# Kernel tuning notes

Hardware: AMD Instinct MI355X
Metric: run time of the kernel (lower is better)

## Reference

```python
import jax, jax.numpy as jnp
import numpy as np

B, T, D, H = 4, 1024, 1024, 16
HD = D // H
DFF = 2048          # ExpertTier hidden width
K = 3               # ConvTier causal kernel size
NEG = -1e9


def layernorm(x, w, b, eps=1e-5):
    m = jnp.mean(x, axis=-1, keepdims=True)
    v = jnp.var(x, axis=-1, keepdims=True)
    return (x - m) * jax.lax.rsqrt(v + eps) * w + b


def rope_cos_sin(t, hd):
    inv = 1.0 / (10000.0 ** (jnp.arange(0, hd, 2, dtype=jnp.float32) / hd))
    freqs = jnp.outer(jnp.arange(t, dtype=jnp.float32), inv)  # (T, hd/2)
    return jnp.cos(freqs), jnp.sin(freqs)


def apply_rope(x, cos, sin):
    # x: (B, H, T, hd); cos/sin: (T, hd/2)
    x1, x2 = jnp.split(x, 2, axis=-1)
    return jnp.concatenate([x1 * cos - x2 * sin, x1 * sin + x2 * cos], axis=-1)


def causal_attn(q, k, v):
    # q,k,v: (..., T, d); full causal softmax attention
    t = q.shape[-2]
    scale = 1.0 / jnp.sqrt(jnp.asarray(q.shape[-1], q.dtype))
    scores = jnp.einsum('...qd,...kd->...qk', q, k) * scale
    mask = jnp.triu(jnp.ones((t, t), dtype=bool), k=1)
    scores = jnp.where(mask, NEG, scores)
    w = jax.nn.softmax(scores, axis=-1)
    return jnp.einsum('...qk,...kd->...qd', w, v)


def setup_inputs() -> dict:
    key = jax.random.key(0)
    ks = jax.random.split(key, 16)
    ws = 0.02
    g = lambda k, shape, s: jax.random.normal(k, shape, dtype=jnp.float32) * s
    return {
        'x': g(ks[0], (B, T, D), 1.0),
        'ln1_w': jnp.ones((D,), jnp.float32), 'ln1_b': jnp.zeros((D,), jnp.float32),
        'qkv_w': g(ks[1], (D, 3 * D), ws),
        'out_w': g(ks[2], (D, D), ws),
        'ln2_w': jnp.ones((D,), jnp.float32), 'ln2_b': jnp.zeros((D,), jnp.float32),
        'router_w': g(ks[3], (D, 4), ws),
        'conv_w': g(ks[4], (D, 1, K), 0.1),             # depthwise OIW, groups=D
        'expert_w1': g(ks[5], (D, DFF), ws),
        'expert_w2': g(ks[6], (DFF, D), ws),
        'at_wq': g(ks[7], (D, D), ws),
        'at_wk': g(ks[8], (D, D), ws),
        'at_wv': g(ks[9], (D, D), ws),
        'at_wo': g(ks[10], (D, D), ws),
        'tier_gate': jnp.full((D,), 0.1, jnp.float32),
        'sink_kv_scale': jnp.asarray(0.1, jnp.float32),
    }


def reference(x, ln1_w, ln1_b, qkv_w, out_w, ln2_w, ln2_b, router_w, conv_w,
              expert_w1, expert_w2, at_wq, at_wk, at_wv, at_wo,
              tier_gate, sink_kv_scale):
    b, t, d = x.shape
    # --- backbone causal self-attention with RoPE (pre-norm) ---
    h1 = layernorm(x, ln1_w, ln1_b)
    qkv = (h1 @ qkv_w).reshape(b, t, 3, H, HD)
    q = qkv[:, :, 0].transpose(0, 2, 1, 3)  # (B,H,T,hd)
    k = qkv[:, :, 1].transpose(0, 2, 1, 3)
    v = qkv[:, :, 2].transpose(0, 2, 1, 3)
    cos, sin = rope_cos_sin(t, HD)
    q = apply_rope(q, cos, sin)
    k = apply_rope(k, cos, sin)
    ao = causal_attn(q, k, v)                         # (B,H,T,hd)
    ao = ao.transpose(0, 2, 1, 3).reshape(b, t, d) @ out_w
    x = x + ao
    # --- router + tiers ---
    h = layernorm(x, ln2_w, ln2_b)
    routing_w = jax.nn.softmax(h @ router_w, axis=-1)  # (B,T,4): conv/expert/attn/sink
    # ConvTier: depthwise causal conv (k=3) + GELU
    hc = jnp.pad(h.transpose(0, 2, 1), ((0, 0), (0, 0), (K - 1, 0)))  # (B,D,T+K-1)
    conv = jax.lax.conv_general_dilated(hc, conv_w, (1,), 'VALID',
                                        feature_group_count=d,
                                        dimension_numbers=('NCH', 'OIH', 'NCH'))
    conv_out = jax.nn.gelu(conv.transpose(0, 2, 1))   # (B,T,D)
    # ExpertTier: 2-layer GELU MLP
    expert_out = jax.nn.gelu(h @ expert_w1) @ expert_w2
    # AttentionTier: single-head causal attention
    attn2 = causal_attn(h @ at_wq, h @ at_wk, h @ at_wv) @ at_wo
    # SinkTier outputs zeros -> contributes nothing to the weighted sum
    combined = (conv_out * routing_w[..., 0:1]
                + expert_out * routing_w[..., 1:2]
                + attn2 * routing_w[..., 2:3])
    x = x + combined * tier_gate
    # sink kv scaling
    kv_scale = 1.0 - routing_w[..., 3] * (1.0 - jnp.abs(sink_kv_scale))
    x = x * kv_scale[..., None]
    return (x, routing_w)
```

## Files before the change

### kernel.cpp

```cpp
#include <hip/hip_runtime.h>

#define Bz 4
#define Tz 1024
#define Dz 1024
#define Hz 16
#define NTz (Bz*Tz)

typedef short s8v __attribute__((ext_vector_type(8)));
typedef float f4v __attribute__((ext_vector_type(4)));

__device__ __forceinline__ float bf2f(unsigned short u){
  unsigned int x = ((unsigned int)u) << 16;
  return __builtin_bit_cast(float, x);
}
__device__ __forceinline__ unsigned short f2bf(float f){
  unsigned int x = __builtin_bit_cast(unsigned int, f);
  x += 0x7fffu + ((x >> 16) & 1u);
  return (unsigned short)(x >> 16);
}
__device__ __forceinline__ float gelu_f(float x){
  float z = 1.5957691216057308f * (x + 0.044715f * x * x * x);
  return x / (1.0f + __expf(-z));
}
__device__ __forceinline__ void gl16(const unsigned short* g, unsigned short* l){
  __builtin_amdgcn_global_load_lds(
      (const __attribute__((address_space(1))) unsigned int*)g,
      (__attribute__((address_space(3))) unsigned int*)l, 16, 0, 0);
}

__global__ __launch_bounds__(256) void k_convtrans(const float* __restrict__ in,
    unsigned short* __restrict__ out, int R, int C)
{
  __shared__ float tile[32][33];
  int c0 = blockIdx.x * 32, r0 = blockIdx.y * 32;
  int tx = threadIdx.x & 31, ty = threadIdx.x >> 5;
  #pragma unroll
  for (int i = 0; i < 32; i += 8)
    tile[ty + i][tx] = in[(long)(r0 + ty + i) * C + c0 + tx];
  __syncthreads();
  #pragma unroll
  for (int i = 0; i < 32; i += 8)
    out[(long)(c0 + ty + i) * R + r0 + tx] = f2bf(tile[tx][ty + i]);
}

__global__ __launch_bounds__(256) void k_convtrans_b(const unsigned short* __restrict__ in,
    unsigned short* __restrict__ out, int ld, long sIn, long sOut)
{
  __shared__ unsigned short tile[32][34];
  in  += (long)blockIdx.z * sIn;
  out += (long)blockIdx.z * sOut;
  int c0 = blockIdx.x * 32, r0 = blockIdx.y * 32;
  int tx = threadIdx.x & 31, ty = threadIdx.x >> 5;
  #pragma unroll
  for (int i = 0; i < 32; i += 8)
    tile[ty + i][tx] = in[(long)(r0 + ty + i) * ld + c0 + tx];
  __syncthreads();
  #pragma unroll
  for (int i = 0; i < 32; i += 8)
    out[(long)(c0 + ty + i) * 1024 + r0 + tx] = tile[tx][ty + i];
}

__global__ __launch_bounds__(256) void k_layernorm(const float* __restrict__ x,
    const float* __restrict__ w, const float* __restrict__ b,
    unsigned short* __restrict__ out)
{
  int row = blockIdx.x, tid = threadIdx.x;
  const float4* xp = (const float4*)(x + (long)row * Dz);
  float4 v = xp[tid];
  float s  = v.x + v.y + v.z + v.w;
  float ss = v.x*v.x + v.y*v.y + v.z*v.z + v.w*v.w;
  int lane = tid & 63, wv = tid >> 6;
  #pragma unroll
  for (int off = 32; off; off >>= 1){ s += __shfl_xor(s, off); ss += __shfl_xor(ss, off); }
  __shared__ float red[8];
  if (lane == 0){ red[wv] = s; red[4 + wv] = ss; }
  __syncthreads();
  s  = red[0] + red[1] + red[2] + red[3];
  ss = red[4] + red[5] + red[6] + red[7];
  float mean = s * (1.0f / Dz);
  float var  = ss * (1.0f / Dz) - mean * mean;
  float rstd = rsqrtf(var + 1e-5f);
  float4 wg = ((const float4*)w)[tid];
  float4 bg = ((const float4*)b)[tid];
  ushort4 ov;
  ov.x = f2bf((v.x - mean) * rstd * wg.x + bg.x);
  ov.y = f2bf((v.y - mean) * rstd * wg.y + bg.y);
  ov.z = f2bf((v.z - mean) * rstd * wg.z + bg.z);
  ov.w = f2bf((v.w - mean) * rstd * wg.w + bg.w);
  *((ushort4*)(out + (long)row * Dz) + tid) = ov;
}

template<int MODE, int BN, bool TRIMAP, bool TRIK, bool DBUF>
__global__ __launch_bounds__(256) void k_gemm(
    const unsigned short* __restrict__ A,
    const unsigned short* __restrict__ Bt,
    float* __restrict__ Cf, unsigned short* __restrict__ Cb,
    const float* __restrict__ addsrc,
    int N, int K, int lda, int ldb,
    long sA, long sB, long sC)
{
  constexpr int BM = 128;
  constexpr int MREP = (BN == 128) ? 4 : 2;
  constexpr int NB = DBUF ? 2 : 1;
  __shared__ unsigned short As[NB][BM * 64];
  __shared__ unsigned short Bs[NB][BN * 64];
  int bm, bn;
  if (TRIMAP) {
    int li = blockIdx.x;
    int r = (int)((sqrtf(4.f * li + 1.f) - 1.f) * 0.5f);
    if ((r + 1) * (r + 2) <= li) ++r;
    if (r * (r + 1) > li) --r;
    bm = r * 128; bn = (li - r * (r + 1)) * BN;
  } else { bm = blockIdx.y * BM; bn = blockIdx.x * BN; }
  A  += (long)blockIdx.z * sA;
  Bt += (long)blockIdx.z * sB;
  int tid = threadIdx.x, w = tid >> 6, lane = tid & 63;
  int wr, wc;
  if (BN == 128) { wr = (w >> 1) * 64; wc = (w & 1) * 64; }
  else           { wr = w * 32;        wc = 0; }
  f4v acc[MREP][4];
  #pragma unroll
  for (int m = 0; m < MREP; ++m)
    #pragma unroll
    for (int n = 0; n < 4; ++n)
      acc[m][n] = (f4v){0.f, 0.f, 0.f, 0.f};

  int Keff = K;
  if (TRIK) Keff = min(K, bm + BM);

  int lrow = lane >> 3;
  int lcol = (((lane & 7) ^ lrow) * 8);
  const unsigned short* AgJ[4];
  int AsOff[4];
  #pragma unroll
  for (int j = 0; j < 4; ++j) {
    AgJ[j] = A + (long)(bm + w * 32 + j * 8 + lrow) * lda + lcol;
    AsOff[j] = (w * 32 + j * 8) * 64;
  }
  constexpr int BCH = BN / 8 / 4;
  const unsigned short* BgJ[BCH];
  int BsOff[BCH];
  #pragma unroll
  for (int j = 0; j < BCH; ++j) {
    BgJ[j] = Bt + (long)(bn + w * (BCH * 8) + j * 8 + lrow) * ldb + lcol;
    BsOff[j] = (w * (BCH * 8) + j * 8) * 64;
  }

  int fr = lane & 15, fg = lane >> 4;
  int sw = (fr & 7) * 8;

  auto stage = [&](int buf, int k0){
    #pragma unroll
    for (int j = 0; j < 4; ++j) gl16(AgJ[j] + k0, &As[buf][AsOff[j]]);
    #pragma unroll
    for (int j = 0; j < BCH; ++j) gl16(BgJ[j] + k0, &Bs[buf][BsOff[j]]);
  };
  auto compute = [&](int buf){
    #pragma unroll
    for (int kk = 0; kk < 2; ++kk) {
      int kg = (kk * 32 + fg * 8) ^ sw;
      s8v af[MREP], bfv[4];
      #pragma unroll
      for (int m = 0; m < MREP; ++m) af[m]  = *(const s8v*)&As[buf][(wr + m * 16 + fr) * 64 + kg];
      #pragma unroll
      for (int n = 0; n < 4; ++n)    bfv[n] = *(const s8v*)&Bs[buf][(wc + n * 16 + fr) * 64 + kg];
      #pragma unroll
      for (int m = 0; m < MREP; ++m)
        #pragma unroll
        for (int n = 0; n < 4; ++n)
          acc[m][n] = __builtin_amdgcn_mfma_f32_16x16x32_bf16(af[m], bfv[n], acc[m][n], 0, 0, 0);
    }
  };

  if (DBUF) {
    int cur = 0;
    stage(0, 0);
    __syncthreads();
    for (int k0 = 0; k0 < Keff; k0 += 64) {
      if (k0 + 64 < Keff) stage(cur ^ 1, k0 + 64);
      compute(cur);
      __syncthreads();
      cur ^= 1;
    }
  } else {
    for (int k0 = 0; k0 < Keff; k0 += 64) {
      __syncthreads();
      stage(0, k0);
      __syncthreads();
      compute(0);
    }
  }

  int cr0 = bm + wr + fg * 4;
  int cc0 = bn + wc + fr;
  #pragma unroll
  for (int m = 0; m < MREP; ++m)
    #pragma unroll
    for (int n = 0; n < 4; ++n)
      #pragma unroll
      for (int i = 0; i < 4; ++i) {
        long row = cr0 + m * 16 + i, col = cc0 + n * 16;
        long idx = (long)blockIdx.z * sC + row * (long)N + col;
        float v = acc[m][n][i];
        if (MODE == 1) v += addsrc[idx];
        if (MODE == 2) v = gelu_f(v);
        if (MODE <= 1) Cf[idx] = v; else Cb[idx] = f2bf(v);
      }
}

__global__ __launch_bounds__(256) void k_qkvsplit(const unsigned short* __restrict__ qkv,
    unsigned short* __restrict__ Qb, unsigned short* __restrict__ Kb,
    unsigned short* __restrict__ Vt)
{
  __shared__ unsigned short vt_s[64][40];
  int t0 = blockIdx.x * 32;
  int bh = blockIdx.y;
  int b = bh >> 4, h = bh & 15;
  int tid = threadIdx.x;
  int tl = tid >> 3, jb = (tid & 7) * 4;
  int t = t0 + tl;
  long base = ((long)(b * Tz + t)) * 3072 + h * 64;
  float cs[4], sn[4];
  #pragma unroll
  for (int ii = 0; ii < 4; ++ii) {
    float inv = exp2f(-(float)(jb + ii) * 0.41524101186092030f);
    sincosf((float)t * inv, &sn[ii], &cs[ii]);
  }
  ushort4 q1 = *(const ushort4*)(qkv + base + jb);
  ushort4 q2 = *(const ushort4*)(qkv + base + jb + 32);
  ushort4 k1 = *(const ushort4*)(qkv + base + 1024 + jb);
  ushort4 k2 = *(const ushort4*)(qkv + base + 1024 + jb + 32);
  ushort4 v1 = *(const ushort4*)(qkv + base + 2048 + jb);
  ushort4 v2 = *(const ushort4*)(qkv + base + 2048 + jb + 32);
  float q1a[4] = {bf2f(q1.x), bf2f(q1.y), bf2f(q1.z), bf2f(q1.w)};
  float q2a[4] = {bf2f(q2.x), bf2f(q2.y), bf2f(q2.z), bf2f(q2.w)};
  float k1a[4] = {bf2f(k1.x), bf2f(k1.y), bf2f(k1.z), bf2f(k1.w)};
  float k2a[4] = {bf2f(k2.x), bf2f(k2.y), bf2f(k2.z), bf2f(k2.w)};
  unsigned short va[4] = {v1.x, v1.y, v1.z, v1.w};
  unsigned short vb[4] = {v2.x, v2.y, v2.z, v2.w};
  unsigned short qo1[4], qo2[4], ko1[4], ko2[4];
  #pragma unroll
  for (int ii = 0; ii < 4; ++ii) {
    qo1[ii] = f2bf((q1a[ii] * cs[ii] - q2a[ii] * sn[ii]) * 0.125f);
    qo2[ii] = f2bf((q1a[ii] * sn[ii] + q2a[ii] * cs[ii]) * 0.125f);
    ko1[ii] = f2bf(k1a[ii] * cs[ii] - k2a[ii] * sn[ii]);
    ko2[ii] = f2bf(k1a[ii] * sn[ii] + k2a[ii] * cs[ii]);
    vt_s[jb + ii][tl]      = va[ii];
    vt_s[jb + 32 + ii][tl] = vb[ii];
  }
  long ob = (long)bh * Tz * 64 + (long)t * 64;
  *(ushort4*)(Qb + ob + jb)      = *(ushort4*)qo1;
  *(ushort4*)(Qb + ob + jb + 32) = *(ushort4*)qo2;
  *(ushort4*)(Kb + ob + jb)      = *(ushort4*)ko1;
  *(ushort4*)(Kb + ob + jb + 32) = *(ushort4*)ko2;
  __syncthreads();
  int d = tid >> 2, tc = (tid & 3) * 8;
  *(uint4*)(Vt + (long)bh * 64 * Tz + (long)d * Tz + t0 + tc) = *(const uint4*)&vt_s[d][tc];
}

__global__ __launch_bounds__(256) void k_attn_mfma(
    const unsigned short* __restrict__ Qb, const unsigned short* __restrict__ Kb,
    const unsigned short* __restrict__ Vt, unsigned short* __restrict__ ao)
{
  __shared__ unsigned short Ks[64][72];
  __shared__ unsigned short Vs[64][72];
  __shared__ unsigned short Ps[4][16][72];
  int qb = 15 - (blockIdx.x >> 6);
  int bh = blockIdx.x & 63;
  int b = bh >> 4, h = bh & 15;
  int t0 = qb * 64;
  int tid = threadIdx.x, w = tid >> 6, lane = tid & 63;
  int fr = lane & 15, fg = lane >> 4;

  const unsigned short* qp = Qb + (long)bh * Tz * 64 + (long)(t0 + w * 16 + fr) * 64 + fg * 8;
  s8v qf[2] = { *(const s8v*)qp, *(const s8v*)(qp + 32) };

  f4v o_acc[4];
  #pragma unroll
  for (int n = 0; n < 4; ++n) o_acc[n] = (f4v){0.f, 0.f, 0.f, 0.f};
  float m_[4] = {-1e30f, -1e30f, -1e30f, -1e30f};
  float l_[4] = {0.f, 0.f, 0.f, 0.f};

  int sr = tid >> 3, sc = (tid & 7) * 8;
  const unsigned short* Kg = Kb + (long)bh * Tz * 64 + (long)sr * 64 + sc;
  const unsigned short* Vg = Vt + (long)bh * 64 * Tz + (long)sr * Tz + sc;

  for (int kt = 0; kt <= qb; ++kt) {
    int k0 = kt * 64;
    __syncthreads();
    *(uint4*)&Ks[sr][sc]      = *(const uint4*)(Kg + (long)k0 * 64);
    *(uint4*)&Ks[sr + 32][sc] = *(const uint4*)(Kg + (long)(k0 + 32) * 64);
    *(uint4*)&Vs[sr][sc]      = *(const uint4*)(Vg + k0);
    *(uint4*)&Vs[sr + 32][sc] = *(const uint4*)(Vg + (long)32 * Tz + k0);
    __syncthreads();

    f4v sacc[4];
    #pragma unroll
    for (int n = 0; n < 4; ++n) sacc[n] = (f4v){0.f, 0.f, 0.f, 0.f};
    #pragma unroll
    for (int kk = 0; kk < 2; ++kk) {
      int kg = kk * 32 + fg * 8;
      #pragma unroll
      for (int n = 0; n < 4; ++n) {
        s8v bf = *(const s8v*)&Ks[n * 16 + fr][kg];
        sacc[n] = __builtin_amdgcn_mfma_f32_16x16x32_bf16(qf[kk], bf, sacc[n], 0, 0, 0);
      }
    }

    bool full = (kt < qb);
    float p[4][4], alpha[4];
    #pragma unroll
    for (int i = 0; i < 4; ++i) {
      int trow = t0 + w * 16 + fg * 4 + i;
      float mx = -1e30f;
      #pragma unroll
      for (int n = 0; n < 4; ++n) {
        float sval = sacc[n][i];
        if (!full) {
          int key = k0 + n * 16 + fr;
          sval = (key <= trow) ? sval : -1e30f;
        }
        p[n][i] = sval;
        mx = fmaxf(mx, sval);
      }
      mx = fmaxf(mx, __shfl_xor(mx, 1));
      mx = fmaxf(mx, __shfl_xor(mx, 2));
      mx = fmaxf(mx, __shfl_xor(mx, 4));
      mx = fmaxf(mx, __shfl_xor(mx, 8));
      float mnew = fmaxf(m_[i], mx);
      alpha[i] = __expf(m_[i] - mnew);
      m_[i] = mnew;
      float ps = 0.f;
      #pragma unroll
      for (int n = 0; n < 4; ++n) {
        float pv = __expf(p[n][i] - mnew);
        p[n][i] = pv;
        ps += pv;
      }
      ps += __shfl_xor(ps, 1); ps += __shfl_xor(ps, 2);
      ps += __shfl_xor(ps, 4); ps += __shfl_xor(ps, 8);
      l_[i] = l_[i] * alpha[i] + ps;
    }
    #pragma unroll
    for (int n = 0; n < 4; ++n)
      #pragma unroll
      for (int i = 0; i < 4; ++i)
        o_acc[n][i] *= alpha[i];
    #pragma unroll
    for (int n = 0; n < 4; ++n)
      #pragma unroll
      for (int i = 0; i < 4; ++i)
        Ps[w][fg * 4 + i][n * 16 + fr] = f2bf(p[n][i]);

    #pragma unroll
    for (int kk = 0; kk < 2; ++kk) {
      int kg = kk * 32 + fg * 8;
      s8v pa = *(const s8v*)&Ps[w][fr][kg];
      #pragma unroll
      for (int n = 0; n < 4; ++n) {
        s8v vb = *(const s8v*)&Vs[n * 16 + fr][kg];
        o_acc[n] = __builtin_amdgcn_mfma_f32_16x16x32_bf16(pa, vb, o_acc[n], 0, 0, 0);
      }
    }
  }

  float inv[4];
  #pragma unroll
  for (int i = 0; i < 4; ++i) inv[i] = 1.0f / l_[i];
  #pragma unroll
  for (int n = 0; n < 4; ++n)
    #pragma unroll
    for (int i = 0; i < 4; ++i) {
      int t = t0 + w * 16 + fg * 4 + i;
      ao[((long)(b * Tz + t)) * Dz + h * 64 + n * 16 + fr] = f2bf(o_acc[n][i] * inv[i]);
    }
}

__global__ __launch_bounds__(256) void k_router(const unsigned short* __restrict__ h,
    const float* __restrict__ rw, float* __restrict__ rout)
{
  int row = blockIdx.x, tid = threadIdx.x;
  float a0 = 0.f, a1 = 0.f, a2 = 0.f, a3 = 0.f;
  const unsigned short* hp = h + (long)row * Dz;
  for (int d = tid; d < Dz; d += 256) {
    float hv = bf2f(hp[d]);
    float4 w4 = *(const float4*)(rw + d * 4);
    a0 = fmaf(hv, w4.x, a0); a1 = fmaf(hv, w4.y, a1);
    a2 = fmaf(hv, w4.z, a2); a3 = fmaf(hv, w4.w, a3);
  }
  int lane = tid & 63, wv = tid >> 6;
  #pragma unroll
  for (int off = 32; off; off >>= 1) {
    a0 += __shfl_xor(a0, off); a1 += __shfl_xor(a1, off);
    a2 += __shfl_xor(a2, off); a3 += __shfl_xor(a3, off);
  }
  __shared__ float red[4][4];
  if (lane == 0){ red[wv][0] = a0; red[wv][1] = a1; red[wv][2] = a2; red[wv][3] = a3; }
  __syncthreads();
  if (tid == 0) {
    float s0 = red[0][0] + red[1][0] + red[2][0] + red[3][0];
    float s1 = red[0][1] + red[1][1] + red[2][1] + red[3][1];
    float s2 = red[0][2] + red[1][2] + red[2][2] + red[3][2];
    float s3 = red[0][3] + red[1][3] + red[2][3] + red[3][3];
    float mx = fmaxf(fmaxf(s0, s1), fmaxf(s2, s3));
    float e0 = __expf(s0 - mx), e1 = __expf(s1 - mx);
    float e2 = __expf(s2 - mx), e3 = __expf(s3 - mx);
    float inv = 1.0f / (e0 + e1 + e2 + e3);
    float4 r = {e0 * inv, e1 * inv, e2 * inv, e3 * inv};
    *(float4*)(rout + (long)row * 4) = r;
  }
}

__global__ __launch_bounds__(256) void k_softmax_causal(const float* __restrict__ S,
    unsigned short* __restrict__ P, float scale)
{
  long row = blockIdx.x;
  int t = (int)(row & (Tz - 1));
  int tid = threadIdx.x;
  const float* sp = S + row * Tz;
  float4 v = *(const float4*)(sp + tid * 4);
  float vv[4];
  vv[0] = (tid*4 + 0 <= t) ? v.x * scale : -1e30f;
  vv[1] = (tid*4 + 1 <= t) ? v.y * scale : -1e30f;
  vv[2] = (tid*4 + 2 <= t) ? v.z * scale : -1e30f;
  vv[3] = (tid*4 + 3 <= t) ? v.w * scale : -1e30f;
  float mx = fmaxf(fmaxf(vv[0], vv[1]), fmaxf(vv[2], vv[3]));
  int lane = tid & 63, wv = tid >> 6;
  #pragma unroll
  for (int off = 32; off; off >>= 1) mx = fmaxf(mx, __shfl_xor(mx, off));
  __shared__ float red[8];
  if (lane == 0) red[wv] = mx;
  __syncthreads();
  mx = fmaxf(fmaxf(red[0], red[1]), fmaxf(red[2], red[3]));
  float p[4];
  float s = 0.f;
  #pragma unroll
  for (int i = 0; i < 4; ++i){ p[i] = __expf(vv[i] - mx); s += p[i]; }
  #pragma unroll
  for (int off = 32; off; off >>= 1) s += __shfl_xor(s, off);
  if (lane == 0) red[4 + wv] = s;
  __syncthreads();
  s = red[4] + red[5] + red[6] + red[7];
  float inv = 1.0f / s;
  ushort4 ov;
  ov.x = f2bf(p[0] * inv); ov.y = f2bf(p[1] * inv);
  ov.z = f2bf(p[2] * inv); ov.w = f2bf(p[3] * inv);
  *((ushort4*)(P + row * Tz) + tid) = ov;
}

__global__ __launch_bounds__(256) void k_combine(
    const float* __restrict__ x2, const unsigned short* __restrict__ hbf,
    const float* __restrict__ eo, const float* __restrict__ ap,
    const float* __restrict__ rout, const float* __restrict__ convw,
    const float* __restrict__ tg, const float* __restrict__ sinkp,
    float* __restrict__ outx)
{
  int row = blockIdx.x, tid = threadIdx.x;
  int t = row & (Tz - 1), b = row >> 10;
  int d0 = tid * 4;
  float4 x4 = *(const float4*)(x2 + (long)row * Dz + d0);
  float4 e4 = *(const float4*)(eo + (long)row * Dz + d0);
  float4 a4 = *(const float4*)(ap + (long)row * Dz + d0);
  float4 t4 = *(const float4*)(tg + d0);
  float4 r4 = *(const float4*)(rout + (long)row * 4);
  float sks = fabsf(sinkp[0]);
  float kv = 1.0f - r4.w * (1.0f - sks);
  const float4* cwp = (const float4*)(convw + (long)d0 * 3);
  float4 c0 = cwp[0], c1 = cwp[1], c2 = cwp[2];
  float cwf[12] = {c0.x, c0.y, c0.z, c0.w, c1.x, c1.y, c1.z, c1.w, c2.x, c2.y, c2.z, c2.w};
  float hv[3][4];
  #pragma unroll
  for (int tap = 0; tap < 3; ++tap) {
    int tt = t - 2 + tap;
    if (tt >= 0) {
      ushort4 hu = *((const ushort4*)(hbf + ((long)(b * Tz + tt)) * Dz + d0));
      hv[tap][0] = bf2f(hu.x); hv[tap][1] = bf2f(hu.y);
      hv[tap][2] = bf2f(hu.z); hv[tap][3] = bf2f(hu.w);
    } else {
      hv[tap][0] = 0.f; hv[tap][1] = 0.f; hv[tap][2] = 0.f; hv[tap][3] = 0.f;
    }
  }
  float ov[4];
  float xi[4] = {x4.x, x4.y, x4.z, x4.w};
  float ei[4] = {e4.x, e4.y, e4.z, e4.w};
  float ai[4] = {a4.x, a4.y, a4.z, a4.w};
  float ti[4] = {t4.x, t4.y, t4.z, t4.w};
  #pragma unroll
  for (int i = 0; i < 4; ++i) {
    float conv = hv[0][i] * cwf[i*3 + 0] + hv[1][i] * cwf[i*3 + 1] + hv[2][i] * cwf[i*3 + 2];
    float comb = gelu_f(conv) * r4.x + ei[i] * r4.y + ai[i] * r4.z;
    ov[i] = (xi[i] + comb * ti[i]) * kv;
  }
  float4 res = {ov[0], ov[1], ov[2], ov[3]};
  *(float4*)(outx + (long)row * Dz + d0) = res;
}

extern "C" void kernel_launch(void* const* d_in, const int* in_sizes, int n_in,
                              void* d_out, int out_size, void* d_ws, size_t ws_size,
                              hipStream_t stream) {
  (void)in_sizes; (void)n_in; (void)out_size; (void)ws_size;
  const float* x       = (const float*)d_in[0];
  const float* ln1_w   = (const float*)d_in[1];
  const float* ln1_b   = (const float*)d_in[2];
  const float* qkv_w   = (const float*)d_in[3];
  const float* out_w   = (const float*)d_in[4];
  const float* ln2_w   = (const float*)d_in[5];
  const float* ln2_b   = (const float*)d_in[6];
  const float* router_w= (const float*)d_in[7];
  const float* conv_w  = (const float*)d_in[8];
  const float* ew1     = (const float*)d_in[9];
  const float* ew2     = (const float*)d_in[10];
  const float* at_wq   = (const float*)d_in[11];
  const float* at_wk   = (const float*)d_in[12];
  const float* at_wv   = (const float*)d_in[13];
  const float* at_wo   = (const float*)d_in[14];
  const float* tg      = (const float*)d_in[15];
  const float* sinkp   = (const float*)d_in[16];
  float* outx = (float*)d_out;
  float* rout = outx + (size_t)NTz * Dz;

  char* ws = (char*)d_ws;
  size_t off = 0;
  auto alloc = [&](size_t bytes) -> char* {
    char* p = ws + off;
    off += (bytes + 255) & ~(size_t)255;
    return p;
  };
  const long TD = (long)Tz * Dz, TT = (long)Tz * Tz;

  unsigned short* w_qkvt  = (unsigned short*)alloc((size_t)3072*1024*2);
  unsigned short* w_outt  = (unsigned short*)alloc((size_t)1024*1024*2);
  unsigned short* w_ew1t  = (unsigned short*)alloc((size_t)2048*1024*2);
  unsigned short* w_ew2t  = (unsigned short*)alloc((size_t)1024*2048*2);
  unsigned short* w_qkv2t = (unsigned short*)alloc((size_t)3072*1024*2);
  unsigned short* w_wot   = (unsigned short*)alloc((size_t)1024*1024*2);
  unsigned short* h1bf    = (unsigned short*)alloc((size_t)NTz*Dz*2);
  unsigned short* qkvb    = (unsigned short*)alloc((size_t)NTz*3072*2);
  unsigned short* aobf    = (unsigned short*)alloc((size_t)NTz*Dz*2);
  float*          x2f     = (float*)alloc((size_t)NTz*Dz*4);
  unsigned short* hbf     = (unsigned short*)alloc((size_t)NTz*Dz*2);
  unsigned short* Pbf     = (unsigned short*)alloc((size_t)Bz*Tz*Tz*2);
  unsigned short* qkv2b   = (unsigned short*)alloc((size_t)NTz*3072*2);
  unsigned short* v2tbf   = (unsigned short*)alloc((size_t)NTz*Dz*2);
  unsigned short* a2obf   = (unsigned short*)alloc((size_t)NTz*Dz*2);
  float*          eof_    = (float*)alloc((size_t)NTz*Dz*4);
  float*          a2pf    = (float*)alloc((size_t)NTz*Dz*4);

  unsigned short* e1bf = qkvb;
  float*          Sf   = (float*)(qkvb + (size_t)8*1024*1024/2 + 4*1024*1024);
  unsigned short* Qb = (unsigned short*)x2f;
  unsigned short* Kb = Pbf;
  unsigned short* Vt = (unsigned short*)a2pf;

  dim3 blk(256);

  k_convtrans<<<dim3(96, 32), blk, 0, stream>>>(qkv_w, w_qkvt, 1024, 3072);
  k_convtrans<<<dim3(32, 32), blk, 0, stream>>>(out_w, w_outt, 1024, 1024);
  k_convtrans<<<dim3(64, 32), blk, 0, stream>>>(ew1,   w_ew1t, 1024, 2048);
  k_convtrans<<<dim3(32, 64), blk, 0, stream>>>(ew2,   w_ew2t, 2048, 1024);
  k_convtrans<<<dim3(32, 32), blk, 0, stream>>>(at_wq, w_qkv2t,               1024, 1024);
  k_convtrans<<<dim3(32, 32), blk, 0, stream>>>(at_wk, w_qkv2t + 1024*1024,   1024, 1024);
  k_convtrans<<<dim3(32, 32), blk, 0, stream>>>(at_wv, w_qkv2t + 2*1024*1024, 1024, 1024);
  k_convtrans<<<dim3(32, 32), blk, 0, stream>>>(at_wo, w_wot, 1024, 1024);

  k_layernorm<<<NTz, blk, 0, stream>>>(x, ln1_w, ln1_b, h1bf);
  k_gemm<3,128,false,false,false><<<dim3(24, 32), blk, 0, stream>>>(h1bf, w_qkvt, nullptr,
      qkvb, nullptr, 3072, 1024, 1024, 1024, 0, 0, 0);
  k_qkvsplit<<<dim3(32, 64), blk, 0, stream>>>(qkvb, Qb, Kb, Vt);
  k_attn_mfma<<<dim3(1024), blk, 0, stream>>>(Qb, Kb, Vt, aobf);
  k_gemm<1,64,false,false,true><<<dim3(16, 32), blk, 0, stream>>>(aobf, w_outt, x2f,
      nullptr, x, 1024, 1024, 1024, 1024, 0, 0, 0);
  k_layernorm<<<NTz, blk, 0, stream>>>(x2f, ln2_w, ln2_b, hbf);
  k_router<<<NTz, blk, 0, stream>>>(hbf, router_w, rout);
  k_gemm<2,128,false,false,false><<<dim3(16, 32), blk, 0, stream>>>(hbf, w_ew1t, nullptr,
      e1bf, nullptr, 2048, 1024, 1024, 1024, 0, 0, 0);
  k_gemm<0,64,false,false,true><<<dim3(16, 32), blk, 0, stream>>>(e1bf, w_ew2t, eof_,
      nullptr, nullptr, 1024, 2048, 2048, 2048, 0, 0, 0);
  k_gemm<3,128,false,false,false><<<dim3(24, 32), blk, 0, stream>>>(hbf, w_qkv2t, nullptr,
      qkv2b, nullptr, 3072, 1024, 1024, 1024, 0, 0, 0);
  k_convtrans_b<<<dim3(32, 32, 4), blk, 0, stream>>>(qkv2b + 2048, v2tbf, 3072,
      (long)Tz*3072, TD);
  k_gemm<0,64,true,false,true><<<dim3(72, 1, 4), blk, 0, stream>>>(qkv2b, qkv2b + 1024, Sf,
      nullptr, nullptr, 1024, 1024, 3072, 3072, (long)Tz*3072, (long)Tz*3072, TT);
  k_softmax_causal<<<NTz, blk, 0, stream>>>(Sf, Pbf, 0.03125f);
  k_gemm<3,64,false,true,true><<<dim3(16, 8, 4), blk, 0, stream>>>(Pbf, v2tbf, nullptr,
      a2obf, nullptr, 1024, 1024, 1024, 1024, TT, TD, TD);
  k_gemm<0,64,false,false,true><<<dim3(16, 32), blk, 0, stream>>>(a2obf, w_wot, a2pf,
      nullptr, nullptr, 1024, 1024, 1024, 1024, 0, 0, 0);
  k_combine<<<NTz, blk, 0, stream>>>(x2f, hbf, eof_, a2pf, rout, conv_w, tg, sinkp, outx);
}
```

Before: 308.9 us.

## Fuse RoPE/QKV split into GEMM epilogue, merge tier GEMMs, swizzle workgroup order

The first QKV GEMM gains an epilogue mode that applies RoPE and scaling and writes Q and K directly in per-head layout, plus V row-major. This removes the separate qkvsplit kernel, and V is transposed by the existing transpose kernel. The expert W1 and attention-tier Q/K/V weights are concatenated into one N=5120 GEMM with GELU applied only to the first 2048 columns, which removes a launch and rereads of the activation. A modulo-8 workgroup index remap is added to all GEMMs, presumably to improve cache locality across XCDs. The costs are an extra V transpose pass, scattered 2-byte epilogue stores, and a separately allocated score buffer.

```diff
diff --git a/kernel.cpp b/kernel.cpp
--- a/kernel.cpp
+++ b/kernel.cpp
@@ -96,6 +96,7 @@
     const unsigned short* __restrict__ Bt,
     float* __restrict__ Cf, unsigned short* __restrict__ Cb,
     const float* __restrict__ addsrc,
+    unsigned short* __restrict__ P1, unsigned short* __restrict__ P2,
     int N, int K, int lda, int ldb,
     long sA, long sB, long sC)
 {
@@ -107,11 +108,18 @@
   int bm, bn;
   if (TRIMAP) {
     int li = blockIdx.x;
+    int nwg = gridDim.x;
+    if ((nwg & 7) == 0) li = (li & 7) * (nwg >> 3) + (li >> 3);
     int r = (int)((sqrtf(4.f * li + 1.f) - 1.f) * 0.5f);
     if ((r + 1) * (r + 2) <= li) ++r;
     if (r * (r + 1) > li) --r;
     bm = r * 128; bn = (li - r * (r + 1)) * BN;
-  } else { bm = blockIdx.y * BM; bn = blockIdx.x * BN; }
+  } else {
+    int lin = blockIdx.y * gridDim.x + blockIdx.x;
+    int nwg = gridDim.x * gridDim.y;
+    if ((nwg & 7) == 0) lin = (lin & 7) * (nwg >> 3) + (lin >> 3);
+    bm = (lin / gridDim.x) * BM; bn = (lin % gridDim.x) * BN;
+  }
   A  += (long)blockIdx.z * sA;
   Bt += (long)blockIdx.z * sB;
   int tid = threadIdx.x, w = tid >> 6, lane = tid & 63;
@@ -193,6 +201,47 @@
 
   int cr0 = bm + wr + fg * 4;
   int cc0 = bn + wc + fr;
+
+  if (MODE == 4) {
+    int sect = bn >> 10;
+    if (sect == 2) {
+      #pragma unroll
+      for (int m = 0; m < MREP; ++m)
+        #pragma unroll
+        for (int n = 0; n < 4; ++n)
+          #pragma unroll
+          for (int i = 0; i < 4; ++i) {
+            int row = cr0 + m * 16 + i;
+            int vcol = (bn - 2048) + wc + n * 16 + fr;
+            P2[(long)row * 1024 + vcol] = f2bf(acc[m][n][i]);
+          }
+    } else {
+      unsigned short* dst = (sect == 0) ? Cb : P1;
+      float scl = (sect == 0) ? 0.125f : 1.0f;
+      int head = ((bn & 1023) + wc) >> 6;
+      float inv0 = exp2f(-(float)fr * 0.4152410118609203f);
+      float inv1 = exp2f(-(float)(fr + 16) * 0.4152410118609203f);
+      #pragma unroll
+      for (int m = 0; m < MREP; ++m)
+        #pragma unroll
+        for (int i = 0; i < 4; ++i) {
+          int row = cr0 + m * 16 + i;
+          int t = row & 1023, bq = row >> 10;
+          float a0 = (float)t * inv0, a1 = (float)t * inv1;
+          float cs0 = __cosf(a0), sn0 = __sinf(a0);
+          float cs1 = __cosf(a1), sn1 = __sinf(a1);
+          float v0 = acc[m][0][i], v1 = acc[m][1][i];
+          float v2 = acc[m][2][i], v3 = acc[m][3][i];
+          long base = ((long)(bq * 16 + head)) * 65536 + (long)t * 64 + fr;
+          dst[base]      = f2bf((v0 * cs0 - v2 * sn0) * scl);
+          dst[base + 32] = f2bf((v0 * sn0 + v2 * cs0) * scl);
+          dst[base + 16] = f2bf((v1 * cs1 - v3 * sn1) * scl);
+          dst[base + 48] = f2bf((v1 * sn1 + v3 * cs1) * scl);
+        }
+    }
+    return;
+  }
+
   #pragma unroll
   for (int m = 0; m < MREP; ++m)
     #pragma unroll
@@ -203,59 +252,9 @@
         long idx = (long)blockIdx.z * sC + row * (long)N + col;
         float v = acc[m][n][i];
         if (MODE == 1) v += addsrc[idx];
-        if (MODE == 2) v = gelu_f(v);
+        if (MODE == 5) { if (col < 2048) v = gelu_f(v); }
         if (MODE <= 1) Cf[idx] = v; else Cb[idx] = f2bf(v);
       }
-}
-
-__global__ __launch_bounds__(256) void k_qkvsplit(const unsigned short* __restrict__ qkv,
-    unsigned short* __restrict__ Qb, unsigned short* __restrict__ Kb,
-    unsigned short* __restrict__ Vt)
-{
-  __shared__ unsigned short vt_s[64][40];
-  int t0 = blockIdx.x * 32;
-  int bh = blockIdx.y;
-  int b = bh >> 4, h = bh & 15;
-  int tid = threadIdx.x;
-  int tl = tid >> 3, jb = (tid & 7) * 4;
-  int t = t0 + tl;
-  long base = ((long)(b * Tz + t)) * 3072 + h * 64;
-  float cs[4], sn[4];
-  #pragma unroll
-  for (int ii = 0; ii < 4; ++ii) {
-    float inv = exp2f(-(float)(jb + ii) * 0.41524101186092030f);
-    sincosf((float)t * inv, &sn[ii], &cs[ii]);
-  }
-  ushort4 q1 = *(const ushort4*)(qkv + base + jb);
-  ushort4 q2 = *(const ushort4*)(qkv + base + jb + 32);
-  ushort4 k1 = *(const ushort4*)(qkv + base + 1024 + jb);
-  ushort4 k2 = *(const ushort4*)(qkv + base + 1024 + jb + 32);
-  ushort4 v1 = *(const ushort4*)(qkv + base + 2048 + jb);
-  ushort4 v2 = *(const ushort4*)(qkv + base + 2048 + jb + 32);
-  float q1a[4] = {bf2f(q1.x), bf2f(q1.y), bf2f(q1.z), bf2f(q1.w)};
-  float q2a[4] = {bf2f(q2.x), bf2f(q2.y), bf2f(q2.z), bf2f(q2.w)};
-  float k1a[4] = {bf2f(k1.x), bf2f(k1.y), bf2f(k1.z), bf2f(k1.w)};
-  float k2a[4] = {bf2f(k2.x), bf2f(k2.y), bf2f(k2.z), bf2f(k2.w)};
-  unsigned short va[4] = {v1.x, v1.y, v1.z, v1.w};
-  unsigned short vb[4] = {v2.x, v2.y, v2.z, v2.w};
-  unsigned short qo1[4], qo2[4], ko1[4], ko2[4];
-  #pragma unroll
-  for (int ii = 0; ii < 4; ++ii) {
-    qo1[ii] = f2bf((q1a[ii] * cs[ii] - q2a[ii] * sn[ii]) * 0.125f);
-    qo2[ii] = f2bf((q1a[ii] * sn[ii] + q2a[ii] * cs[ii]) * 0.125f);
-    ko1[ii] = f2bf(k1a[ii] * cs[ii] - k2a[ii] * sn[ii]);
-    ko2[ii] = f2bf(k1a[ii] * sn[ii] + k2a[ii] * cs[ii]);
-    vt_s[jb + ii][tl]      = va[ii];
-    vt_s[jb + 32 + ii][tl] = vb[ii];
-  }
-  long ob = (long)bh * Tz * 64 + (long)t * 64;
-  *(ushort4*)(Qb + ob + jb)      = *(ushort4*)qo1;
-  *(ushort4*)(Qb + ob + jb + 32) = *(ushort4*)qo2;
-  *(ushort4*)(Kb + ob + jb)      = *(ushort4*)ko1;
-  *(ushort4*)(Kb + ob + jb + 32) = *(ushort4*)ko2;
-  __syncthreads();
-  int d = tid >> 2, tc = (tid & 3) * 8;
-  *(uint4*)(Vt + (long)bh * 64 * Tz + (long)d * Tz + t0 + tc) = *(const uint4*)&vt_s[d][tc];
 }
 
 __global__ __launch_bounds__(256) void k_attn_mfma(
@@ -530,62 +529,59 @@
 
   unsigned short* w_qkvt  = (unsigned short*)alloc((size_t)3072*1024*2);
   unsigned short* w_outt  = (unsigned short*)alloc((size_t)1024*1024*2);
-  unsigned short* w_ew1t  = (unsigned short*)alloc((size_t)2048*1024*2);
+  unsigned short* w_tiert = (unsigned short*)alloc((size_t)5120*1024*2);
   unsigned short* w_ew2t  = (unsigned short*)alloc((size_t)1024*2048*2);
-  unsigned short* w_qkv2t = (unsigned short*)alloc((size_t)3072*1024*2);
   unsigned short* w_wot   = (unsigned short*)alloc((size_t)1024*1024*2);
   unsigned short* h1bf    = (unsigned short*)alloc((size_t)NTz*Dz*2);
-  unsigned short* qkvb    = (unsigned short*)alloc((size_t)NTz*3072*2);
+  unsigned short* tierb   = (unsigned short*)alloc((size_t)NTz*5120*2);
   unsigned short* aobf    = (unsigned short*)alloc((size_t)NTz*Dz*2);
   float*          x2f     = (float*)alloc((size_t)NTz*Dz*4);
   unsigned short* hbf     = (unsigned short*)alloc((size_t)NTz*Dz*2);
   unsigned short* Pbf     = (unsigned short*)alloc((size_t)Bz*Tz*Tz*2);
-  unsigned short* qkv2b   = (unsigned short*)alloc((size_t)NTz*3072*2);
   unsigned short* v2tbf   = (unsigned short*)alloc((size_t)NTz*Dz*2);
   unsigned short* a2obf   = (unsigned short*)alloc((size_t)NTz*Dz*2);
   float*          eof_    = (float*)alloc((size_t)NTz*Dz*4);
   float*          a2pf    = (float*)alloc((size_t)NTz*Dz*4);
-
-  unsigned short* e1bf = qkvb;
-  float*          Sf   = (float*)(qkvb + (size_t)8*1024*1024/2 + 4*1024*1024);
+  float*          Sf      = (float*)alloc((size_t)Bz*Tz*Tz*4);
+
   unsigned short* Qb = (unsigned short*)x2f;
   unsigned short* Kb = Pbf;
+  unsigned short* Vb = tierb;
   unsigned short* Vt = (unsigned short*)a2pf;
 
   dim3 blk(256);
 
   k_convtrans<<<dim3(96, 32), blk, 0, stream>>>(qkv_w, w_qkvt, 1024, 3072);
   k_convtrans<<<dim3(32, 32), blk, 0, stream>>>(out_w, w_outt, 1024, 1024);
-  k_convtrans<<<dim3(64, 32), blk, 0, stream>>>(ew1,   w_ew1t, 1024, 2048);
+  k_convtrans<<<dim3(64, 32), blk, 0, stream>>>(ew1,   w_tiert,                 1024, 2048);
+  k_convtrans<<<dim3(32, 32), blk, 0, stream>>>(at_wq, w_tiert + 2048*1024,     1024, 1024);
+  k_convtrans<<<dim3(32, 32), blk, 0, stream>>>(at_wk, w_tiert + 3072*1024,     1024, 1024);
+  k_convtrans<<<dim3(32, 32), blk, 0, stream>>>(at_wv, w_tiert + (size_t)4096*1024, 1024, 1024);
   k_convtrans<<<dim3(32, 64), blk, 0, stream>>>(ew2,   w_ew2t, 2048, 1024);
-  k_convtrans<<<dim3(32, 32), blk, 0, stream>>>(at_wq, w_qkv2t,               1024, 1024);
-  k_convtrans<<<dim3(32, 32), blk, 0, stream>>>(at_wk, w_qkv2t + 1024*1024,   1024, 1024);
-  k_convtrans<<<dim3(32, 32), blk, 0, stream>>>(at_wv, w_qkv2t + 2*1024*1024, 1024, 1024);
   k_convtrans<<<dim3(32, 32), blk, 0, stream>>>(at_wo, w_wot, 1024, 1024);
 
   k_layernorm<<<NTz, blk, 0, stream>>>(x, ln1_w, ln1_b, h1bf);
-  k_gemm<3,128,false,false,false><<<dim3(24, 32), blk, 0, stream>>>(h1bf, w_qkvt, nullptr,
-      qkvb, nullptr, 3072, 1024, 1024, 1024, 0, 0, 0);
-  k_qkvsplit<<<dim3(32, 64), blk, 0, stream>>>(qkvb, Qb, Kb, Vt);
+  k_gemm<4,128,false,false,false><<<dim3(24, 32), blk, 0, stream>>>(h1bf, w_qkvt,
+      nullptr, Qb, nullptr, Kb, Vb, 3072, 1024, 1024, 1024, 0, 0, 0);
+  k_convtrans_b<<<dim3(32, 32, 4), blk, 0, stream>>>(Vb, Vt, 1024, TD, TD);
   k_attn_mfma<<<dim3(1024), blk, 0, stream>>>(Qb, Kb, Vt, aobf);
   k_gemm<1,64,false,false,true><<<dim3(16, 32), blk, 0, stream>>>(aobf, w_outt, x2f,
-      nullptr, x, 1024, 1024, 1024, 1024, 0, 0, 0);
+      nullptr, x, nullptr, nullptr, 1024, 1024, 1024, 1024, 0, 0, 0);
   k_layernorm<<<NTz, blk, 0, stream>>>(x2f, ln2_w, ln2_b, hbf);
   k_router<<<NTz, blk, 0, stream>>>(hbf, router_w, rout);
-  k_gemm<2,128,false,false,false><<<dim3(16, 32), blk, 0, stream>>>(hbf, w_ew1t, nullptr,
-      e1bf, nullptr, 2048, 1024, 1024, 1024, 0, 0, 0);
-  k_gemm<0,64,false,false,true><<<dim3(16, 32), blk, 0, stream>>>(e1bf, w_ew2t, eof_,
-      nullptr, nullptr, 1024, 2048, 2048, 2048, 0, 0, 0);
-  k_gemm<3,128,false,false,false><<<dim3(24, 32), blk, 0, stream>>>(hbf, w_qkv2t, nullptr,
-      qkv2b, nullptr, 3072, 1024, 1024, 1024, 0, 0, 0);
-  k_convtrans_b<<<dim3(32, 32, 4), blk, 0, stream>>>(qkv2b + 2048, v2tbf, 3072,
-      (long)Tz*3072, TD);
-  k_gemm<0,64,true,false,true><<<dim3(72, 1, 4), blk, 0, stream>>>(qkv2b, qkv2b + 1024, Sf,
-      nullptr, nullptr, 1024, 1024, 3072, 3072, (long)Tz*3072, (long)Tz*3072, TT);
+  k_gemm<5,128,false,false,false><<<dim3(40, 32), blk, 0, stream>>>(hbf, w_tiert,
+      nullptr, tierb, nullptr, nullptr, nullptr, 5120, 1024, 1024, 1024, 0, 0, 0);
+  k_gemm<0,64,false,false,true><<<dim3(16, 32), blk, 0, stream>>>(tierb, w_ew2t, eof_,
+      nullptr, nullptr, nullptr, nullptr, 1024, 2048, 5120, 2048, 0, 0, 0);
+  k_convtrans_b<<<dim3(32, 32, 4), blk, 0, stream>>>(tierb + 4096, v2tbf, 5120,
+      (long)Tz*5120, TD);
+  k_gemm<0,64,true,false,true><<<dim3(72, 1, 4), blk, 0, stream>>>(tierb + 2048,
+      tierb + 3072, Sf, nullptr, nullptr, nullptr, nullptr,
+      1024, 1024, 5120, 5120, (long)Tz*5120, (long)Tz*5120, TT);
   k_softmax_causal<<<NTz, blk, 0, stream>>>(Sf, Pbf, 0.03125f);
   k_gemm<3,64,false,true,true><<<dim3(16, 8, 4), blk, 0, stream>>>(Pbf, v2tbf, nullptr,
-      a2obf, nullptr, 1024, 1024, 1024, 1024, TT, TD, TD);
+      a2obf, nullptr, nullptr, nullptr, 1024, 1024, 1024, 1024, TT, TD, TD);
   k_gemm<0,64,false,false,true><<<dim3(16, 32), blk, 0, stream>>>(a2obf, w_wot, a2pf,
-      nullptr, nullptr, 1024, 1024, 1024, 1024, 0, 0, 0);
+      nullptr, nullptr, nullptr, nullptr, 1024, 1024, 1024, 1024, 0, 0, 0);
   k_combine<<<NTz, blk, 0, stream>>>(x2f, hbf, eof_, a2pf, rout, conv_w, tg, sinkp, outx);
 }
```

Result: no change. 313.5 us (+1.5%).
